# Optimization experiments

Measured on AMD Instinct MI355X. Metric: run time of the kernel, lower is better.

The kernel has to match this reference:

```python
import jax, jax.numpy as jnp
import numpy as np

D_MODEL = 1024
NUM_HEADS = 16
DEPTH = D_MODEL // NUM_HEADS


def setup_inputs() -> dict:
    key = jax.random.key(0)
    ks = jax.random.split(key, 12)
    B, S = 4, 2048
    scale = 1.0 / np.sqrt(D_MODEL)
    inp = {
        "query": jax.random.normal(ks[0], (B, S, D_MODEL), dtype=jnp.float32),
        "key": jax.random.normal(ks[1], (B, S, D_MODEL), dtype=jnp.float32),
        "value": jax.random.normal(ks[2], (B, S, D_MODEL), dtype=jnp.float32),
        "mask": jnp.zeros((B, 1, 1, S), dtype=jnp.float32),  # 1.0 = masked position
        "Wq": jax.random.normal(ks[3], (D_MODEL, D_MODEL), dtype=jnp.float32) * scale,
        "bq": jnp.zeros((D_MODEL,), dtype=jnp.float32),
        "Wk": jax.random.normal(ks[4], (D_MODEL, D_MODEL), dtype=jnp.float32) * scale,
        "bk": jnp.zeros((D_MODEL,), dtype=jnp.float32),
        "Wv": jax.random.normal(ks[5], (D_MODEL, D_MODEL), dtype=jnp.float32) * scale,
        "bv": jnp.zeros((D_MODEL,), dtype=jnp.float32),
        "Wo": jax.random.normal(ks[6], (D_MODEL, D_MODEL), dtype=jnp.float32) * scale,
        "bo": jnp.zeros((D_MODEL,), dtype=jnp.float32),
    }
    return inp


def _split_heads(x):
    # [B, S, D] -> [B, H, S, depth]
    B, S, _ = x.shape
    return x.reshape(B, S, NUM_HEADS, DEPTH).transpose(0, 2, 1, 3)


def reference(query, key, value, mask, Wq, bq, Wk, bk, Wv, bv, Wo, bo):
    B, Sq, _ = query.shape
    q = _split_heads(query @ Wq + bq)   # [B, H, Sq, d]
    k = _split_heads(key @ Wk + bk)     # [B, H, Sk, d]
    v = _split_heads(value @ Wv + bv)   # [B, H, Sk, d]
    logits = jnp.einsum('bhqd,bhkd->bhqk', q, k) / jnp.sqrt(jnp.float32(DEPTH))
    logits = logits + mask * (-1e9)
    attn = jax.nn.softmax(logits, axis=-1)
    ctx = jnp.einsum('bhqk,bhkd->bhqd', attn, v)        # [B, H, Sq, d]
    ctx = ctx.transpose(0, 2, 1, 3).reshape(B, Sq, D_MODEL)
    return ctx @ Wo + bo
```

## Files before the change

kernel.cpp:

```cpp
#include <hip/hip_runtime.h>
#include <math.h>

#define BB 4
#define SS 2048
#define DDM 1024
#define HH 16
#define MM (BB * SS)

typedef _Float16 f16;
typedef f16 half8 __attribute__((ext_vector_type(8)));
typedef f16 f16x4 __attribute__((ext_vector_type(4)));
typedef float f32x4 __attribute__((ext_vector_type(4)));

#define GLOAD16(g, l)                                                  \
  __builtin_amdgcn_global_load_lds(                                    \
      (const __attribute__((address_space(1))) void*)(g),              \
      (__attribute__((address_space(3))) void*)(l), 16, 0, 0)

__global__ void cvt_f16_k(const float* __restrict__ in, f16* __restrict__ out,
                          int n4) {
  int i = blockIdx.x * blockDim.x + threadIdx.x;
  const int stride = gridDim.x * blockDim.x;
  for (; i < n4; i += stride) {
    const float4 v = reinterpret_cast<const float4*>(in)[i];
    f16x4 o;
    o.x = (f16)v.x; o.y = (f16)v.y; o.z = (f16)v.z; o.w = (f16)v.w;
    reinterpret_cast<f16x4*>(out)[i] = o;
  }
}

__global__ void wtr_k(const float* __restrict__ W, f16* __restrict__ Wt) {
  __shared__ float t[32][33];
  const int bx = blockIdx.x * 32, by = blockIdx.y * 32;
  const int tx = threadIdx.x, ty = threadIdx.y;
#pragma unroll
  for (int i = 0; i < 4; ++i)
    t[ty + i * 8][tx] = W[(size_t)(by + ty + i * 8) * DDM + bx + tx];
  __syncthreads();
#pragma unroll
  for (int i = 0; i < 4; ++i)
    Wt[(size_t)(bx + ty + i * 8) * DDM + by + tx] = (f16)t[tx][ty + i * 8];
}

__global__ __launch_bounds__(256, 2) void gemm_f16_k(
    const f16* __restrict__ A, const f16* __restrict__ Bt,
    const float* __restrict__ bias, void* __restrict__ out, int mode) {
  __shared__ f16 Al[128 * 32];
  __shared__ f16 Bl[128 * 32];
  const int tid = threadIdx.x;
  const int l = tid & 63, w = tid >> 6;
  const int lr = l & 15, lg = l >> 4;
  const int wr = w >> 1, wc = w & 1;
  const int bm = blockIdx.x << 7, bn = blockIdx.y << 7;

  f32x4 acc[4][4];
#pragma unroll
  for (int m = 0; m < 4; ++m)
#pragma unroll
    for (int n = 0; n < 4; ++n) acc[m][n] = (f32x4){0.f, 0.f, 0.f, 0.f};

  const int c0 = tid, c1 = 256 + tid;
  const f16* Ap0 = A + (size_t)(bm + (c0 >> 2)) * DDM + (c0 & 3) * 8;
  const f16* Ap1 = A + (size_t)(bm + (c1 >> 2)) * DDM + (c1 & 3) * 8;
  const f16* Bp0 = Bt + (size_t)(bn + (c0 >> 2)) * DDM + (c0 & 3) * 8;
  const f16* Bp1 = Bt + (size_t)(bn + (c1 >> 2)) * DDM + (c1 & 3) * 8;
  f16* AlU0 = Al + (w * 64) * 8;
  f16* AlU1 = Al + (256 + w * 64) * 8;
  f16* BlU0 = Bl + (w * 64) * 8;
  f16* BlU1 = Bl + (256 + w * 64) * 8;

  for (int kk = 0; kk < DDM; kk += 32) {
    GLOAD16(Ap0 + kk, AlU0);
    GLOAD16(Ap1 + kk, AlU1);
    GLOAD16(Bp0 + kk, BlU0);
    GLOAD16(Bp1 + kk, BlU1);
    __syncthreads();
    half8 af[4], bf[4];
#pragma unroll
    for (int m = 0; m < 4; ++m)
      af[m] = *reinterpret_cast<const half8*>(
          Al + (wr * 64 + m * 16 + lr) * 32 + lg * 8);
#pragma unroll
    for (int n = 0; n < 4; ++n)
      bf[n] = *reinterpret_cast<const half8*>(
          Bl + (wc * 64 + n * 16 + lr) * 32 + lg * 8);
#pragma unroll
    for (int m = 0; m < 4; ++m)
#pragma unroll
      for (int n = 0; n < 4; ++n)
        acc[m][n] = __builtin_amdgcn_mfma_f32_16x16x32_f16(af[m], bf[n],
                                                           acc[m][n], 0, 0, 0);
    __syncthreads();
  }

#pragma unroll
  for (int n = 0; n < 4; ++n) {
    const int gn = bn + wc * 64 + n * 16 + lr;
    const float bv = bias[gn];
#pragma unroll
    for (int m = 0; m < 4; ++m) {
#pragma unroll
      for (int r = 0; r < 4; ++r) {
        const int gm = bm + wr * 64 + m * 16 + lg * 4 + r;
        const float v = acc[m][n][r] + bv;
        if (mode == 0) {
          reinterpret_cast<float*>(out)[(size_t)gm * DDM + gn] = v;
        } else {
          const int b = gm >> 11, s = gm & (SS - 1);
          const int h = gn >> 6, d = gn & 63;
          reinterpret_cast<f16*>(
              out)[(((size_t)(b * HH + h) * SS + s) << 6) + d] = (f16)v;
        }
      }
    }
  }
}

__global__ __launch_bounds__(256, 2) void attn_f16_k(
    const f16* __restrict__ Q, const f16* __restrict__ K,
    const f16* __restrict__ V, const float* __restrict__ mask,
    f16* __restrict__ ctx) {
  __shared__ f16 Kl[64 * 64];
  __shared__ f16 Vl[64 * 72];
  __shared__ f16 Pl[4 * 16 * 72];
  __shared__ float Ml[SS];

  const int tid = threadIdx.x;
  const int l = tid & 63, w = tid >> 6;
  const int lr = l & 15, lg = l >> 4;
  const int qt = blockIdx.x;
  const int bh = blockIdx.y;
  const int b = bh >> 4, h = bh & 15;

  for (int i = tid; i < SS; i += 256) Ml[i] = mask[(size_t)b * SS + i] * -1e9f;

  const size_t qrow = (size_t)bh * SS + qt * 64 + w * 16 + lr;
  half8 qf0 = *reinterpret_cast<const half8*>(Q + qrow * 64 + lg * 8);
  half8 qf1 = *reinterpret_cast<const half8*>(Q + qrow * 64 + 32 + lg * 8);

  float m_s[4], l_s[4];
  f32x4 oa[4];
#pragma unroll
  for (int r = 0; r < 4; ++r) { m_s[r] = -1e30f; l_s[r] = 0.f; }
#pragma unroll
  for (int n = 0; n < 4; ++n) oa[n] = (f32x4){0.f, 0.f, 0.f, 0.f};

  const f16* Kg = K + (size_t)bh * SS * 64;
  const f16* Vg = V + (size_t)bh * SS * 64;

  const int c0 = tid, c1 = 256 + tid;
  f16* KlU0 = Kl + (w * 64) * 8;
  f16* KlU1 = Kl + (256 + w * 64) * 8;
  const int vkey0 = c0 >> 3, vd00 = (c0 & 7) * 8;
  const int vkey1 = c1 >> 3, vd01 = (c1 & 7) * 8;
  f16* Pw = Pl + w * (16 * 72);

  for (int kt = 0; kt < 32; ++kt) {
    __syncthreads();
    const f16* Kt = Kg + (size_t)kt * 64 * 64;
    GLOAD16(Kt + (size_t)c0 * 8, KlU0);
    GLOAD16(Kt + (size_t)c1 * 8, KlU1);
    const f16* Vtg = Vg + (size_t)kt * 64 * 64;
    uint4 v0 = *reinterpret_cast<const uint4*>(Vtg + vkey0 * 64 + vd00);
    uint4 v1 = *reinterpret_cast<const uint4*>(Vtg + vkey1 * 64 + vd01);
    {
      const f16* p0 = reinterpret_cast<const f16*>(&v0);
      const f16* p1 = reinterpret_cast<const f16*>(&v1);
#pragma unroll
      for (int j = 0; j < 8; ++j) Vl[(vd00 + j) * 72 + vkey0] = p0[j];
#pragma unroll
      for (int j = 0; j < 8; ++j) Vl[(vd01 + j) * 72 + vkey1] = p1[j];
    }
    __syncthreads();

    f32x4 sv[4];
#pragma unroll
    for (int n = 0; n < 4; ++n) {
      f32x4 s = (f32x4){0.f, 0.f, 0.f, 0.f};
      half8 kf0 = *reinterpret_cast<const half8*>(
          Kl + (n * 16 + lr) * 64 + lg * 8);
      half8 kf1 = *reinterpret_cast<const half8*>(
          Kl + (n * 16 + lr) * 64 + 32 + lg * 8);
      s = __builtin_amdgcn_mfma_f32_16x16x32_f16(qf0, kf0, s, 0, 0, 0);
      s = __builtin_amdgcn_mfma_f32_16x16x32_f16(qf1, kf1, s, 0, 0, 0);
      const float mk = Ml[kt * 64 + n * 16 + lr];
#pragma unroll
      for (int r = 0; r < 4; ++r) sv[n][r] = s[r] * 0.125f + mk;
    }

#pragma unroll
    for (int r = 0; r < 4; ++r) {
      float mx = fmaxf(fmaxf(sv[0][r], sv[1][r]), fmaxf(sv[2][r], sv[3][r]));
      mx = fmaxf(mx, __shfl_xor(mx, 1));
      mx = fmaxf(mx, __shfl_xor(mx, 2));
      mx = fmaxf(mx, __shfl_xor(mx, 4));
      mx = fmaxf(mx, __shfl_xor(mx, 8));
      const float mn = fmaxf(m_s[r], mx);
      const float corr = __expf(m_s[r] - mn);
      float sum = 0.f;
#pragma unroll
      for (int n = 0; n < 4; ++n) {
        const float p = __expf(sv[n][r] - mn);
        sv[n][r] = p;
        sum += p;
      }
      sum += __shfl_xor(sum, 1);
      sum += __shfl_xor(sum, 2);
      sum += __shfl_xor(sum, 4);
      sum += __shfl_xor(sum, 8);
      l_s[r] = l_s[r] * corr + sum;
      m_s[r] = mn;
#pragma unroll
      for (int n = 0; n < 4; ++n) oa[n][r] *= corr;
    }

#pragma unroll
    for (int n = 0; n < 4; ++n)
#pragma unroll
      for (int r = 0; r < 4; ++r)
        Pw[(lg * 4 + r) * 72 + n * 16 + lr] = (f16)sv[n][r];

    half8 pa0 = *reinterpret_cast<const half8*>(Pw + lr * 72 + lg * 8);
    half8 pa1 = *reinterpret_cast<const half8*>(Pw + lr * 72 + 32 + lg * 8);
#pragma unroll
    for (int n = 0; n < 4; ++n) {
      half8 vf0 = *reinterpret_cast<const half8*>(
          Vl + (n * 16 + lr) * 72 + lg * 8);
      half8 vf1 = *reinterpret_cast<const half8*>(
          Vl + (n * 16 + lr) * 72 + 32 + lg * 8);
      oa[n] = __builtin_amdgcn_mfma_f32_16x16x32_f16(pa0, vf0, oa[n], 0, 0, 0);
      oa[n] = __builtin_amdgcn_mfma_f32_16x16x32_f16(pa1, vf1, oa[n], 0, 0, 0);
    }
  }

#pragma unroll
  for (int r = 0; r < 4; ++r) {
    const float inv = 1.0f / l_s[r];
    const int s_g = qt * 64 + w * 16 + lg * 4 + r;
#pragma unroll
    for (int n = 0; n < 4; ++n)
      ctx[((size_t)b * SS + s_g) * DDM + h * 64 + n * 16 + lr] =
          (f16)(oa[n][r] * inv);
  }
}

extern "C" void kernel_launch(void* const* d_in, const int* in_sizes, int n_in,
                              void* d_out, int out_size, void* d_ws,
                              size_t ws_size, hipStream_t stream) {
  const float* query = (const float*)d_in[0];
  const float* key   = (const float*)d_in[1];
  const float* value = (const float*)d_in[2];
  const float* mask  = (const float*)d_in[3];
  const float* Wq = (const float*)d_in[4];
  const float* bq = (const float*)d_in[5];
  const float* Wk = (const float*)d_in[6];
  const float* bk = (const float*)d_in[7];
  const float* Wv = (const float*)d_in[8];
  const float* bv = (const float*)d_in[9];
  const float* Wo = (const float*)d_in[10];
  const float* bo = (const float*)d_in[11];
  float* out = (float*)d_out;

  const size_t E = (size_t)MM * DDM;
  f16* ws = (f16*)d_ws;
  f16* Qh = ws;
  f16* Kh = Qh + E;
  f16* Vh = Kh + E;
  f16* Wt0 = Vh + E;
  f16* Wt1 = Wt0 + (size_t)DDM * DDM;
  f16* Wt2 = Wt1 + (size_t)DDM * DDM;
  f16* Wt3 = Wt2 + (size_t)DDM * DDM;
  f16* Qp = Wt3 + (size_t)DDM * DDM;
  f16* Kp = Qp + E;
  f16* Vp = Kp + E;
  f16* Ch = Vp + E;

  const int n4 = (int)(E / 4);
  cvt_f16_k<<<2048, 256, 0, stream>>>(query, Qh, n4);
  cvt_f16_k<<<2048, 256, 0, stream>>>(key, Kh, n4);
  cvt_f16_k<<<2048, 256, 0, stream>>>(value, Vh, n4);
  dim3 tb(32, 8), tg(32, 32);
  wtr_k<<<tg, tb, 0, stream>>>(Wq, Wt0);
  wtr_k<<<tg, tb, 0, stream>>>(Wk, Wt1);
  wtr_k<<<tg, tb, 0, stream>>>(Wv, Wt2);
  wtr_k<<<tg, tb, 0, stream>>>(Wo, Wt3);

  dim3 gg(MM / 128, DDM / 128);
  gemm_f16_k<<<gg, 256, 0, stream>>>(Qh, Wt0, bq, Qp, 1);
  gemm_f16_k<<<gg, 256, 0, stream>>>(Kh, Wt1, bk, Kp, 1);
  gemm_f16_k<<<gg, 256, 0, stream>>>(Vh, Wt2, bv, Vp, 1);
  attn_f16_k<<<dim3(SS / 64, BB * HH), 256, 0, stream>>>(Qp, Kp, Vp, mask, Ch);
  gemm_f16_k<<<gg, 256, 0, stream>>>(Ch, Wt3, bo, out, 0);
}
```

Measured before the change: 626.5 us.

## Swizzle LDS layouts and double GEMM K-tile to cut bank conflicts

The GEMM kernel now stages a 64-wide K slice per iteration instead of 32. Its shared-memory tiles are written and read with an XOR swizzle of the 16-byte column chunk by row, which halves the number of barrier pairs and is meant to avoid LDS bank conflicts. The attention kernel applies the same XOR swizzle to the K tile and shrinks the V/P row padding from 72 to 66 halves. The 66-half stride leaves the 16-byte vector LDS reads unaligned, which risks split accesses or correctness issues, and the larger GEMM tile doubles its shared-memory use.

```diff
diff --git a/kernel.cpp b/kernel.cpp
--- a/kernel.cpp
+++ b/kernel.cpp
@@ -45,8 +45,8 @@
 __global__ __launch_bounds__(256, 2) void gemm_f16_k(
     const f16* __restrict__ A, const f16* __restrict__ Bt,
     const float* __restrict__ bias, void* __restrict__ out, int mode) {
-  __shared__ f16 Al[128 * 32];
-  __shared__ f16 Bl[128 * 32];
+  __shared__ f16 Al[128 * 64];
+  __shared__ f16 Bl[128 * 64];
   const int tid = threadIdx.x;
   const int l = tid & 63, w = tid >> 6;
   const int lr = l & 15, lg = l >> 4;
@@ -59,37 +59,42 @@
 #pragma unroll
     for (int n = 0; n < 4; ++n) acc[m][n] = (f32x4){0.f, 0.f, 0.f, 0.f};
 
-  const int c0 = tid, c1 = 256 + tid;
-  const f16* Ap0 = A + (size_t)(bm + (c0 >> 2)) * DDM + (c0 & 3) * 8;
-  const f16* Ap1 = A + (size_t)(bm + (c1 >> 2)) * DDM + (c1 & 3) * 8;
-  const f16* Bp0 = Bt + (size_t)(bn + (c0 >> 2)) * DDM + (c0 & 3) * 8;
-  const f16* Bp1 = Bt + (size_t)(bn + (c1 >> 2)) * DDM + (c1 & 3) * 8;
-  f16* AlU0 = Al + (w * 64) * 8;
-  f16* AlU1 = Al + (256 + w * 64) * 8;
-  f16* BlU0 = Bl + (w * 64) * 8;
-  f16* BlU1 = Bl + (256 + w * 64) * 8;
-
-  for (int kk = 0; kk < DDM; kk += 32) {
-    GLOAD16(Ap0 + kk, AlU0);
-    GLOAD16(Ap1 + kk, AlU1);
-    GLOAD16(Bp0 + kk, BlU0);
-    GLOAD16(Bp1 + kk, BlU1);
+  const int srow = tid >> 3;
+  const int scol = (tid & 7) ^ (srow & 7);
+  const f16* Ap = A + (size_t)(bm + srow) * DDM + scol * 8;
+  const f16* Bp = Bt + (size_t)(bn + srow) * DDM + scol * 8;
+
+  for (int kk = 0; kk < DDM; kk += 64) {
+#pragma unroll
+    for (int it = 0; it < 4; ++it) {
+      GLOAD16(Ap + (size_t)(it * 32) * DDM + kk, Al + (it * 256 + w * 64) * 8);
+      GLOAD16(Bp + (size_t)(it * 32) * DDM + kk, Bl + (it * 256 + w * 64) * 8);
+    }
     __syncthreads();
-    half8 af[4], bf[4];
-#pragma unroll
-    for (int m = 0; m < 4; ++m)
-      af[m] = *reinterpret_cast<const half8*>(
-          Al + (wr * 64 + m * 16 + lr) * 32 + lg * 8);
-#pragma unroll
-    for (int n = 0; n < 4; ++n)
-      bf[n] = *reinterpret_cast<const half8*>(
-          Bl + (wc * 64 + n * 16 + lr) * 32 + lg * 8);
-#pragma unroll
-    for (int m = 0; m < 4; ++m)
-#pragma unroll
-      for (int n = 0; n < 4; ++n)
-        acc[m][n] = __builtin_amdgcn_mfma_f32_16x16x32_f16(af[m], bf[n],
-                                                           acc[m][n], 0, 0, 0);
+    half8 af[2][4], bf[2][4];
+#pragma unroll
+    for (int kh = 0; kh < 2; ++kh) {
+#pragma unroll
+      for (int m = 0; m < 4; ++m) {
+        const int row = wr * 64 + m * 16 + lr;
+        af[kh][m] = *reinterpret_cast<const half8*>(
+            Al + row * 64 + (((kh * 4 + lg) ^ (lr & 7)) * 8));
+      }
+#pragma unroll
+      for (int n = 0; n < 4; ++n) {
+        const int row = wc * 64 + n * 16 + lr;
+        bf[kh][n] = *reinterpret_cast<const half8*>(
+            Bl + row * 64 + (((kh * 4 + lg) ^ (lr & 7)) * 8));
+      }
+    }
+#pragma unroll
+    for (int kh = 0; kh < 2; ++kh)
+#pragma unroll
+      for (int m = 0; m < 4; ++m)
+#pragma unroll
+        for (int n = 0; n < 4; ++n)
+          acc[m][n] = __builtin_amdgcn_mfma_f32_16x16x32_f16(
+              af[kh][m], bf[kh][n], acc[m][n], 0, 0, 0);
     __syncthreads();
   }
 
@@ -121,8 +126,8 @@
     const f16* __restrict__ V, const float* __restrict__ mask,
     f16* __restrict__ ctx) {
   __shared__ f16 Kl[64 * 64];
-  __shared__ f16 Vl[64 * 72];
-  __shared__ f16 Pl[4 * 16 * 72];
+  __shared__ f16 Vl[64 * 66];
+  __shared__ f16 Pl[4 * 16 * 66];
   __shared__ float Ml[SS];
 
   const int tid = threadIdx.x;
@@ -148,18 +153,22 @@
   const f16* Kg = K + (size_t)bh * SS * 64;
   const f16* Vg = V + (size_t)bh * SS * 64;
 
-  const int c0 = tid, c1 = 256 + tid;
+  const int srow = tid >> 3;
+  const int scol = (tid & 7) ^ (srow & 7);
   f16* KlU0 = Kl + (w * 64) * 8;
   f16* KlU1 = Kl + (256 + w * 64) * 8;
+  const int c0 = tid, c1 = 256 + tid;
   const int vkey0 = c0 >> 3, vd00 = (c0 & 7) * 8;
   const int vkey1 = c1 >> 3, vd01 = (c1 & 7) * 8;
-  f16* Pw = Pl + w * (16 * 72);
+  f16* Pw = Pl + w * (16 * 66);
+
+  const int kx = lr & 7;
 
   for (int kt = 0; kt < 32; ++kt) {
     __syncthreads();
     const f16* Kt = Kg + (size_t)kt * 64 * 64;
-    GLOAD16(Kt + (size_t)c0 * 8, KlU0);
-    GLOAD16(Kt + (size_t)c1 * 8, KlU1);
+    GLOAD16(Kt + srow * 64 + scol * 8, KlU0);
+    GLOAD16(Kt + (32 + srow) * 64 + scol * 8, KlU1);
     const f16* Vtg = Vg + (size_t)kt * 64 * 64;
     uint4 v0 = *reinterpret_cast<const uint4*>(Vtg + vkey0 * 64 + vd00);
     uint4 v1 = *reinterpret_cast<const uint4*>(Vtg + vkey1 * 64 + vd01);
@@ -167,9 +176,9 @@
       const f16* p0 = reinterpret_cast<const f16*>(&v0);
       const f16* p1 = reinterpret_cast<const f16*>(&v1);
 #pragma unroll
-      for (int j = 0; j < 8; ++j) Vl[(vd00 + j) * 72 + vkey0] = p0[j];
-#pragma unroll
-      for (int j = 0; j < 8; ++j) Vl[(vd01 + j) * 72 + vkey1] = p1[j];
+      for (int j = 0; j < 8; ++j) Vl[(vd00 + j) * 66 + vkey0] = p0[j];
+#pragma unroll
+      for (int j = 0; j < 8; ++j) Vl[(vd01 + j) * 66 + vkey1] = p1[j];
     }
     __syncthreads();
 
@@ -177,10 +186,11 @@
 #pragma unroll
     for (int n = 0; n < 4; ++n) {
       f32x4 s = (f32x4){0.f, 0.f, 0.f, 0.f};
+      const int krow = (n * 16 + lr) * 64;
       half8 kf0 = *reinterpret_cast<const half8*>(
-          Kl + (n * 16 + lr) * 64 + lg * 8);
+          Kl + krow + ((lg ^ kx) * 8));
       half8 kf1 = *reinterpret_cast<const half8*>(
-          Kl + (n * 16 + lr) * 64 + 32 + lg * 8);
+          Kl + krow + (((4 + lg) ^ kx) * 8));
       s = __builtin_amdgcn_mfma_f32_16x16x32_f16(qf0, kf0, s, 0, 0, 0);
       s = __builtin_amdgcn_mfma_f32_16x16x32_f16(qf1, kf1, s, 0, 0, 0);
       const float mk = Ml[kt * 64 + n * 16 + lr];
@@ -218,16 +228,16 @@
     for (int n = 0; n < 4; ++n)
 #pragma unroll
       for (int r = 0; r < 4; ++r)
-        Pw[(lg * 4 + r) * 72 + n * 16 + lr] = (f16)sv[n][r];
-
-    half8 pa0 = *reinterpret_cast<const half8*>(Pw + lr * 72 + lg * 8);
-    half8 pa1 = *reinterpret_cast<const half8*>(Pw + lr * 72 + 32 + lg * 8);
+        Pw[(lg * 4 + r) * 66 + n * 16 + lr] = (f16)sv[n][r];
+
+    half8 pa0 = *reinterpret_cast<const half8*>(Pw + lr * 66 + lg * 8);
+    half8 pa1 = *reinterpret_cast<const half8*>(Pw + lr * 66 + 32 + lg * 8);
 #pragma unroll
     for (int n = 0; n < 4; ++n) {
       half8 vf0 = *reinterpret_cast<const half8*>(
-          Vl + (n * 16 + lr) * 72 + lg * 8);
+          Vl + (n * 16 + lr) * 66 + lg * 8);
       half8 vf1 = *reinterpret_cast<const half8*>(
-          Vl + (n * 16 + lr) * 72 + 32 + lg * 8);
+          Vl + (n * 16 + lr) * 66 + 32 + lg * 8);
       oa[n] = __builtin_amdgcn_mfma_f32_16x16x32_f16(pa0, vf0, oa[n], 0, 0, 0);
       oa[n] = __builtin_amdgcn_mfma_f32_16x16x32_f16(pa1, vf1, oa[n], 0, 0, 0);
     }
```

Result: faster. 574.6 us (-8.3%).
